# Optimization experiments

Measured on AMD Instinct MI355X. Metric: run time of the kernel, lower is better.

## Reference

```python
import jax, jax.numpy as jnp
import numpy as np

N = 262144   # occupied sparse voxels
C = 64       # channels
K3 = 27      # 3^3 kernel offsets (rulebook width)


def spconv(feats, W, nbr):
    """Submanifold sparse conv: gather -> matmul -> accumulate per kernel offset.
    feats: [N, Cin], W: [K3, Cin, Cout], nbr: [N, K3] int32 neighbor indices.
    """
    def step(acc, wi):
        w, idx = wi          # w: [Cin, Cout], idx: [N]
        return acc + feats[idx] @ w, None
    acc = jnp.zeros((feats.shape[0], W.shape[-1]), dtype=feats.dtype)
    out, _ = jax.lax.scan(step, acc, (W, nbr.T))
    return out


def inr(feats, nbr, w00, w01, w10, w11, w12):
    # branch 0: conv0_1(relu(conv0_0(x)))  (both k=3)
    out0 = spconv(jax.nn.relu(spconv(feats, w00, nbr)), w01, nbr)
    # branch 1: conv1_2(relu(conv1_1(relu(conv1_0(x)))))  (1x1, k=3, 1x1)
    out1 = jax.nn.relu(spconv(jax.nn.relu(feats @ w10), w11, nbr)) @ w12
    # concat halves back to C, residual add
    return jnp.concatenate([out0, out1], axis=1) + feats


def setup_inputs() -> dict:
    key = jax.random.key(0)
    ks = jax.random.split(key, 16)
    Ch = C // 2
    s3 = 1.0 / np.sqrt(K3 * C)
    s3h = 1.0 / np.sqrt(K3 * Ch)
    s1 = 1.0 / np.sqrt(C)
    s1h = 1.0 / np.sqrt(Ch)
    feats = jax.random.normal(ks[0], (N, C), dtype=jnp.float32)
    nbr = jax.random.randint(ks[1], (N, K3), 0, N, dtype=jnp.int32)
    w1 = jax.random.normal(ks[2], (K3, C, C), dtype=jnp.float32) * s3
    w2 = jax.random.normal(ks[3], (K3, C, C), dtype=jnp.float32) * s3
    # 3 stacked INR blocks
    b00 = jax.random.normal(ks[4], (3, K3, C, Ch), dtype=jnp.float32) * s3
    b01 = jax.random.normal(ks[5], (3, K3, Ch, Ch), dtype=jnp.float32) * s3h
    b10 = jax.random.normal(ks[6], (3, C, Ch), dtype=jnp.float32) * s1
    b11 = jax.random.normal(ks[7], (3, K3, Ch, Ch), dtype=jnp.float32) * s3h
    b12 = jax.random.normal(ks[8], (3, Ch, Ch), dtype=jnp.float32) * s1h
    return {"feats": feats, "nbr": nbr, "w1": w1, "w2": w2,
            "b00": b00, "b01": b01, "b10": b10, "b11": b11, "b12": b12}


def reference(feats, nbr, w1, w2, b00, b01, b10, b11, b12):
    x = jax.nn.relu(spconv(feats, w1, nbr))   # x = relu(conv1(x))
    h = x
    for i in range(3):
        h = inr(h, nbr, b00[i], b01[i], b10[i], b11[i], b12[i])
    out = h + x                                # block(x) + x
    return spconv(out, w2, nbr)                # conv2(out)
```

## Files before the change

### kernel.cpp

```cpp
#include <hip/hip_runtime.h>
#include <hip/hip_bf16.h>

typedef __attribute__((ext_vector_type(8))) __bf16 bf16x8;
typedef __attribute__((ext_vector_type(4))) float f32x4;

#define DEVI __device__ __forceinline__

static constexpr int NVOX = 262144;

DEVI unsigned short f2b_rne(float f) {
    unsigned int u = __float_as_uint(f);
    u = (u + 0x7fffu + ((u >> 16) & 1u)) >> 16;
    return (unsigned short)u;
}
DEVI float b2f(unsigned short h) {
    return __uint_as_float(((unsigned int)h) << 16);
}
DEVI bf16x8 ld8(const unsigned short* p) { return *reinterpret_cast<const bf16x8*>(p); }
DEVI f32x4 mfma16(bf16x8 a, bf16x8 b, f32x4 c) {
    return __builtin_amdgcn_mfma_f32_16x16x32_bf16(a, b, c, 0, 0, 0);
}

DEVI void stage16(const unsigned short* __restrict__ src, unsigned short* dst,
                  int n16, int tid, int nthr) {
    const float4* s = reinterpret_cast<const float4*>(src);
    float4* d = reinterpret_cast<float4*>(dst);
    for (int c = tid; c < n16; c += nthr) d[c] = s[c];
}


__global__ void f2b_kernel(const float* __restrict__ src, unsigned short* __restrict__ dst) {
    const size_t i = (size_t)(blockIdx.x * 256 + threadIdx.x) * 8;
    const float4 a = *reinterpret_cast<const float4*>(src + i);
    const float4 b = *reinterpret_cast<const float4*>(src + i + 4);
    union { unsigned short h[8]; uint4 v; } o;
    o.h[0] = f2b_rne(a.x); o.h[1] = f2b_rne(a.y); o.h[2] = f2b_rne(a.z); o.h[3] = f2b_rne(a.w);
    o.h[4] = f2b_rne(b.x); o.h[5] = f2b_rne(b.y); o.h[6] = f2b_rne(b.z); o.h[7] = f2b_rne(b.w);
    *reinterpret_cast<uint4*>(dst + i) = o.v;
}

__global__ void wconv_kernel(const float* __restrict__ src, unsigned short* __restrict__ dst,
                             int K, int Cin, int Cout) {
    const int KC = Cin >> 5, NT = Cout >> 4;
    const int total = K * KC * NT * 512;
    src += (size_t)blockIdx.y * K * Cin * Cout;
    dst += (size_t)blockIdx.y * total;
    for (int e = blockIdx.x * 256 + threadIdx.x; e < total; e += gridDim.x * 256) {
        const int j = e & 7;
        const int ln = (e >> 3) & 63;
        const int blob = e >> 9;
        const int nt = blob % NT;
        const int t = blob / NT;
        const int kc = t % KC;
        const int k = t / KC;
        const int cin = kc * 32 + (ln >> 4) * 8 + j;
        const int cout = nt * 16 + (ln & 15);
        dst[e] = f2b_rne(src[((size_t)k * Cin + cin) * Cout + cout]);
    }
}


template<bool RELU, bool OUTF32>
__global__ __launch_bounds__(1024)
void conv_full_kernel(const unsigned short* __restrict__ in,
                      const int* __restrict__ nbr,
                      const unsigned short* __restrict__ wf,
                      void* __restrict__ outv)
{
    __shared__ unsigned short wlds[14 * 8 * 512];
    const int tid = threadIdx.x;
    const int lane = tid & 63, wave = tid >> 6;
    const int lrow = lane & 15, lkg = lane >> 4;
    const int vb = blockIdx.x * 512 + wave * 32;

    constexpr int ID = 6;
    constexpr int GS = 3;

    const int* nrow0 = nbr + (size_t)(vb + lrow) * 27;
    const int* nrow1 = nbr + (size_t)(vb + 16 + lrow) * 27;

    int i0[ID], i1[ID];
    bf16x8 ga[GS][2][2];

#pragma unroll
    for (int t = 0; t < ID; ++t) { i0[t] = nrow0[t]; i1[t] = nrow1[t]; }
#pragma unroll
    for (int t = 0; t < 2; ++t) {
        const unsigned short* a0 = in + (size_t)i0[t] * 64 + lkg * 8;
        const unsigned short* a1 = in + (size_t)i1[t] * 64 + lkg * 8;
        ga[t][0][0] = ld8(a0); ga[t][0][1] = ld8(a0 + 32);
        ga[t][1][0] = ld8(a1); ga[t][1][1] = ld8(a1 + 32);
    }

    stage16(wf, wlds, 14 * 8 * 64, tid, 1024);

    const f32x4 FZ = {0.f, 0.f, 0.f, 0.f};
    f32x4 acc[2][4];
#pragma unroll
    for (int m = 0; m < 2; ++m)
#pragma unroll
        for (int nt = 0; nt < 4; ++nt) acc[m][nt] = FZ;

    __syncthreads();

#pragma unroll
    for (int t = 0; t < 27; ++t) {
        if (t == 14) {
            __syncthreads();
            stage16(wf + (size_t)14 * 8 * 512, wlds, 13 * 8 * 64, tid, 1024);
            __syncthreads();
        }
        if (t + ID < 27) {
            i0[t % ID] = nrow0[t + ID];
            i1[t % ID] = nrow1[t + ID];
        }
        if (t + 2 < 27) {
            const int u = t + 2, s = u % GS;
            const unsigned short* a0 = in + (size_t)i0[u % ID] * 64 + lkg * 8;
            const unsigned short* a1 = in + (size_t)i1[u % ID] * 64 + lkg * 8;
            ga[s][0][0] = ld8(a0); ga[s][0][1] = ld8(a0 + 32);
            ga[s][1][0] = ld8(a1); ga[s][1][1] = ld8(a1 + 32);
        }
        const int kk = (t < 14) ? t : t - 14;
        const unsigned short* bl = wlds + kk * 8 * 512 + lane * 8;
        const int s = t % GS;
#pragma unroll
        for (int kc = 0; kc < 2; ++kc)
#pragma unroll
            for (int nt = 0; nt < 4; ++nt) {
                const bf16x8 bf = ld8(bl + (kc * 4 + nt) * 512);
                acc[0][nt] = mfma16(ga[s][0][kc], bf, acc[0][nt]);
                acc[1][nt] = mfma16(ga[s][1][kc], bf, acc[1][nt]);
            }
    }

#pragma unroll
    for (int m = 0; m < 2; ++m)
#pragma unroll
        for (int nt = 0; nt < 4; ++nt)
#pragma unroll
            for (int r = 0; r < 4; ++r) {
                const int v = vb + m * 16 + lkg * 4 + r;
                float val = acc[m][nt][r];
                if (RELU) val = fmaxf(val, 0.f);
                if (OUTF32)
                    reinterpret_cast<float*>(outv)[(size_t)v * 64 + nt * 16 + lrow] = val;
                else
                    reinterpret_cast<unsigned short*>(outv)[(size_t)v * 64 + nt * 16 + lrow] = f2b_rne(val);
            }
}

__global__ __launch_bounds__(1024)
void kernel_A(const unsigned short* __restrict__ h,
              const int* __restrict__ nbr,
              const unsigned short* __restrict__ b00f,
              const unsigned short* __restrict__ b10f,
              unsigned short* __restrict__ u)
{
    __shared__ unsigned short wlds[(27 * 4 + 4) * 512];
    const int tid = threadIdx.x;
    const int lane = tid & 63, wave = tid >> 6;
    const int lrow = lane & 15, lkg = lane >> 4;
    const int vb = blockIdx.x * 512 + wave * 32;

    constexpr int ID = 6;
    constexpr int GS = 3;

    const int* nrow0 = nbr + (size_t)(vb + lrow) * 27;
    const int* nrow1 = nbr + (size_t)(vb + 16 + lrow) * 27;

    int i0[ID], i1[ID];
    bf16x8 ga[GS][2][2];

#pragma unroll
    for (int t = 0; t < ID; ++t) { i0[t] = nrow0[t]; i1[t] = nrow1[t]; }
#pragma unroll
    for (int t = 0; t < 2; ++t) {
        const unsigned short* a0 = h + (size_t)i0[t] * 64 + lkg * 8;
        const unsigned short* a1 = h + (size_t)i1[t] * 64 + lkg * 8;
        ga[t][0][0] = ld8(a0); ga[t][0][1] = ld8(a0 + 32);
        ga[t][1][0] = ld8(a1); ga[t][1][1] = ld8(a1 + 32);
    }

    stage16(b00f, wlds, 27 * 4 * 64, tid, 1024);
    stage16(b10f, wlds + 27 * 4 * 512, 4 * 64, tid, 1024);

    const f32x4 FZ = {0.f, 0.f, 0.f, 0.f};
    f32x4 acc0[2][2], acc1[2][2];
#pragma unroll
    for (int m = 0; m < 2; ++m)
#pragma unroll
        for (int nt = 0; nt < 2; ++nt) { acc0[m][nt] = FZ; acc1[m][nt] = FZ; }

    __syncthreads();

#pragma unroll
    for (int t = 0; t < 27; ++t) {
        if (t + ID < 27) {
            i0[t % ID] = nrow0[t + ID];
            i1[t % ID] = nrow1[t + ID];
        }
        if (t + 2 < 27) {
            const int u2 = t + 2, s = u2 % GS;
            const unsigned short* a0 = h + (size_t)i0[u2 % ID] * 64 + lkg * 8;
            const unsigned short* a1 = h + (size_t)i1[u2 % ID] * 64 + lkg * 8;
            ga[s][0][0] = ld8(a0); ga[s][0][1] = ld8(a0 + 32);
            ga[s][1][0] = ld8(a1); ga[s][1][1] = ld8(a1 + 32);
        }
        const unsigned short* bl = wlds + t * 4 * 512 + lane * 8;
        const int s = t % GS;
#pragma unroll
        for (int kc = 0; kc < 2; ++kc)
#pragma unroll
            for (int nt = 0; nt < 2; ++nt) {
                const bf16x8 bf = ld8(bl + (kc * 2 + nt) * 512);
                acc0[0][nt] = mfma16(ga[s][0][kc], bf, acc0[0][nt]);
                acc0[1][nt] = mfma16(ga[s][1][kc], bf, acc0[1][nt]);
            }
    }
    {
        const unsigned short* bl = wlds + 27 * 4 * 512 + lane * 8;
#pragma unroll
        for (int m = 0; m < 2; ++m) {
            const unsigned short* ar = h + (size_t)(vb + m * 16 + lrow) * 64;
#pragma unroll
            for (int kc = 0; kc < 2; ++kc) {
                const bf16x8 af = ld8(ar + kc * 32 + lkg * 8);
#pragma unroll
                for (int nt = 0; nt < 2; ++nt) {
                    const bf16x8 bf = ld8(bl + (kc * 2 + nt) * 512);
                    acc1[m][nt] = mfma16(af, bf, acc1[m][nt]);
                }
            }
        }
    }
#pragma unroll
    for (int m = 0; m < 2; ++m)
#pragma unroll
        for (int nt = 0; nt < 2; ++nt)
#pragma unroll
            for (int r = 0; r < 4; ++r) {
                const int v = vb + m * 16 + lkg * 4 + r;
                u[(size_t)v * 64 + nt * 16 + lrow] = f2b_rne(fmaxf(acc0[m][nt][r], 0.f));
                u[(size_t)v * 64 + 32 + nt * 16 + lrow] = f2b_rne(fmaxf(acc1[m][nt][r], 0.f));
            }
}

__global__ __launch_bounds__(1024)
void kernel_B(const unsigned short* __restrict__ u,
              const int* __restrict__ nbr,
              const unsigned short* __restrict__ b01f,
              const unsigned short* __restrict__ b11f,
              const unsigned short* __restrict__ b12f,
              const unsigned short* __restrict__ hres,
              const unsigned short* __restrict__ xres,
              unsigned short* __restrict__ hout)
{
    __shared__ unsigned short wlds[110 * 512];
    __shared__ unsigned short t2lds[16][512];
    const int tid = threadIdx.x;
    const int lane = tid & 63, wave = tid >> 6;
    const int lrow = lane & 15, lkg = lane >> 4;
    const int vb = blockIdx.x * 512 + wave * 32;

    constexpr int ID = 6;
    constexpr int GS = 3;

    const int* nrow0 = nbr + (size_t)(vb + lrow) * 27;
    const int* nrow1 = nbr + (size_t)(vb + 16 + lrow) * 27;

    int i0[ID], i1[ID];
    bf16x8 ga[GS][2][2];

#pragma unroll
    for (int t = 0; t < ID; ++t) { i0[t] = nrow0[t]; i1[t] = nrow1[t]; }
#pragma unroll
    for (int t = 0; t < 2; ++t) {
        const unsigned short* a0 = u + (size_t)i0[t] * 64 + lkg * 8;
        const unsigned short* a1 = u + (size_t)i1[t] * 64 + lkg * 8;
        ga[t][0][0] = ld8(a0); ga[t][0][1] = ld8(a0 + 32);
        ga[t][1][0] = ld8(a1); ga[t][1][1] = ld8(a1 + 32);
    }

    stage16(b01f, wlds, 54 * 64, tid, 1024);
    stage16(b11f, wlds + 54 * 512, 54 * 64, tid, 1024);
    stage16(b12f, wlds + 108 * 512, 2 * 64, tid, 1024);

    const f32x4 FZ = {0.f, 0.f, 0.f, 0.f};
    f32x4 acc0[2][2], acc1[2][2];
#pragma unroll
    for (int m = 0; m < 2; ++m)
#pragma unroll
        for (int nt = 0; nt < 2; ++nt) { acc0[m][nt] = FZ; acc1[m][nt] = FZ; }

    __syncthreads();

#pragma unroll
    for (int t = 0; t < 27; ++t) {
        if (t + ID < 27) {
            i0[t % ID] = nrow0[t + ID];
            i1[t % ID] = nrow1[t + ID];
        }
        if (t + 2 < 27) {
            const int u2 = t + 2, s = u2 % GS;
            const unsigned short* a0 = u + (size_t)i0[u2 % ID] * 64 + lkg * 8;
            const unsigned short* a1 = u + (size_t)i1[u2 % ID] * 64 + lkg * 8;
            ga[s][0][0] = ld8(a0); ga[s][0][1] = ld8(a0 + 32);
            ga[s][1][0] = ld8(a1); ga[s][1][1] = ld8(a1 + 32);
        }
        const unsigned short* bl = wlds + lane * 8;
        const int s = t % GS;
#pragma unroll
        for (int nt = 0; nt < 2; ++nt) {
            const bf16x8 w01 = ld8(bl + (t * 2 + nt) * 512);
            const bf16x8 w11 = ld8(bl + (54 + t * 2 + nt) * 512);
            acc0[0][nt] = mfma16(ga[s][0][0], w01, acc0[0][nt]);
            acc0[1][nt] = mfma16(ga[s][1][0], w01, acc0[1][nt]);
            acc1[0][nt] = mfma16(ga[s][0][1], w11, acc1[0][nt]);
            acc1[1][nt] = mfma16(ga[s][1][1], w11, acc1[1][nt]);
        }
    }

    f32x4 out1[2][2];
    char* tb = reinterpret_cast<char*>(&t2lds[wave][0]);
#pragma unroll
    for (int m = 0; m < 2; ++m) {
#pragma unroll
        for (int nt = 0; nt < 2; ++nt)
#pragma unroll
            for (int r = 0; r < 4; ++r) {
                const int row = lkg * 4 + r;
                const int byte = (nt * 16 + lrow) * 2;
                const int off = row * 64 + (((byte >> 4) ^ (row & 3)) << 4) + (byte & 15);
                *reinterpret_cast<unsigned short*>(tb + off) = f2b_rne(fmaxf(acc1[m][nt][r], 0.f));
            }
        __syncthreads();
        const int roff = lrow * 64 + ((lkg ^ (lrow & 3)) << 4);
        const bf16x8 af2 = *reinterpret_cast<const bf16x8*>(tb + roff);
#pragma unroll
        for (int nt = 0; nt < 2; ++nt) {
            const bf16x8 w12 = ld8(wlds + (108 + nt) * 512 + lane * 8);
            out1[m][nt] = mfma16(af2, w12, FZ);
        }
        __syncthreads();
    }

#pragma unroll
    for (int m = 0; m < 2; ++m)
#pragma unroll
        for (int nt = 0; nt < 2; ++nt)
#pragma unroll
            for (int r = 0; r < 4; ++r) {
                const int v = vb + m * 16 + lkg * 4 + r;
                const int c0 = nt * 16 + lrow;
                const int c1 = 32 + c0;
                float r0 = acc0[m][nt][r] + b2f(hres[(size_t)v * 64 + c0]);
                float r1 = out1[m][nt][r] + b2f(hres[(size_t)v * 64 + c1]);
                if (xres) {
                    r0 += b2f(xres[(size_t)v * 64 + c0]);
                    r1 += b2f(xres[(size_t)v * 64 + c1]);
                }
                hout[(size_t)v * 64 + c0] = f2b_rne(r0);
                hout[(size_t)v * 64 + c1] = f2b_rne(r1);
            }
}


extern "C" void kernel_launch(void* const* d_in, const int* in_sizes, int n_in,
                              void* d_out, int out_size, void* d_ws, size_t ws_size,
                              hipStream_t stream)
{
    const float* feats = (const float*)d_in[0];
    const int*   nbr   = (const int*)d_in[1];
    const float* w1    = (const float*)d_in[2];
    const float* w2    = (const float*)d_in[3];
    const float* b00   = (const float*)d_in[4];
    const float* b01   = (const float*)d_in[5];
    const float* b10   = (const float*)d_in[6];
    const float* b11   = (const float*)d_in[7];
    const float* b12   = (const float*)d_in[8];

    const size_t NC = (size_t)NVOX * 64;
    unsigned short* xbuf = (unsigned short*)d_ws;
    unsigned short* hbuf = xbuf + NC;
    unsigned short* wbuf = hbuf + NC;
    if (ws_size < (2 * NC + 562176) * sizeof(unsigned short)) return;

    unsigned short* fbuf = (unsigned short*)d_out;
    unsigned short* ubuf = fbuf + NC;

    const size_t OFF_W1 = 0, OFF_W2 = 110592, OFF_B00 = 221184, OFF_B01 = 387072,
                 OFF_B10 = 470016, OFF_B11 = 476160, OFF_B12 = 559104;

    f2b_kernel<<<8192, 256, 0, stream>>>(feats, fbuf);
    wconv_kernel<<<dim3(432, 1), 256, 0, stream>>>(w1, wbuf + OFF_W1, 27, 64, 64);
    wconv_kernel<<<dim3(432, 1), 256, 0, stream>>>(w2, wbuf + OFF_W2, 27, 64, 64);
    wconv_kernel<<<dim3(216, 3), 256, 0, stream>>>(b00, wbuf + OFF_B00, 27, 64, 32);
    wconv_kernel<<<dim3(108, 3), 256, 0, stream>>>(b01, wbuf + OFF_B01, 27, 32, 32);
    wconv_kernel<<<dim3(8, 3),   256, 0, stream>>>(b10, wbuf + OFF_B10, 1, 64, 32);
    wconv_kernel<<<dim3(108, 3), 256, 0, stream>>>(b11, wbuf + OFF_B11, 27, 32, 32);
    wconv_kernel<<<dim3(4, 3),   256, 0, stream>>>(b12, wbuf + OFF_B12, 1, 32, 32);

    conv_full_kernel<true, false><<<512, 1024, 0, stream>>>(fbuf, nbr, wbuf + OFF_W1, xbuf);

    for (int i = 0; i < 3; ++i) {
        kernel_A<<<512, 1024, 0, stream>>>(i ? hbuf : xbuf, nbr,
                                           wbuf + OFF_B00 + (size_t)i * 55296,
                                           wbuf + OFF_B10 + (size_t)i * 2048, ubuf);
        kernel_B<<<512, 1024, 0, stream>>>(ubuf, nbr,
                                           wbuf + OFF_B01 + (size_t)i * 27648,
                                           wbuf + OFF_B11 + (size_t)i * 27648,
                                           wbuf + OFF_B12 + (size_t)i * 1024,
                                           i ? hbuf : xbuf,
                                           (i == 2) ? xbuf : (const unsigned short*)nullptr,
                                           hbuf);
    }

    conv_full_kernel<false, true><<<512, 1024, 0, stream>>>(hbuf, nbr, wbuf + OFF_W2, d_out);
}
```

Baseline: 1.174 ms.

## Shrink LDS weight footprint with chunked staging to raise occupancy

Each conv kernel now stages its weights into LDS in smaller chunks (7 offsets, or two halves of 14 and 13) instead of the whole 27-offset set, and kernel_B reuses the weight buffer as its transpose scratch and reads the 1x1 weights from global memory into registers. Launch bounds now request more waves per EU. The aim is to cut per-block LDS use so more 1024-thread blocks fit per CU and hide gather latency better. The cost is extra barriers and restaging inside the main loop, which stall every wave while a chunk loads, plus tighter register limits that could cause spills.

```diff
diff --git a/kernel.cpp b/kernel.cpp
--- a/kernel.cpp
+++ b/kernel.cpp
@@ -61,13 +61,13 @@
 
 
 template<bool RELU, bool OUTF32>
-__global__ __launch_bounds__(1024)
+__global__ __launch_bounds__(1024, 8)
 void conv_full_kernel(const unsigned short* __restrict__ in,
                       const int* __restrict__ nbr,
                       const unsigned short* __restrict__ wf,
                       void* __restrict__ outv)
 {
-    __shared__ unsigned short wlds[14 * 8 * 512];
+    __shared__ unsigned short wlds[7 * 8 * 512];
     const int tid = threadIdx.x;
     const int lane = tid & 63, wave = tid >> 6;
     const int lrow = lane & 15, lkg = lane >> 4;
@@ -92,8 +92,6 @@
         ga[t][1][0] = ld8(a1); ga[t][1][1] = ld8(a1 + 32);
     }
 
-    stage16(wf, wlds, 14 * 8 * 64, tid, 1024);
-
     const f32x4 FZ = {0.f, 0.f, 0.f, 0.f};
     f32x4 acc[2][4];
 #pragma unroll
@@ -101,13 +99,12 @@
 #pragma unroll
         for (int nt = 0; nt < 4; ++nt) acc[m][nt] = FZ;
 
-    __syncthreads();
-
 #pragma unroll
     for (int t = 0; t < 27; ++t) {
-        if (t == 14) {
-            __syncthreads();
-            stage16(wf + (size_t)14 * 8 * 512, wlds, 13 * 8 * 64, tid, 1024);
+        if (t % 7 == 0) {
+            const int nk = (27 - t) < 7 ? (27 - t) : 7;
+            __syncthreads();
+            stage16(wf + (size_t)t * 8 * 512, wlds, nk * 8 * 64, tid, 1024);
             __syncthreads();
         }
         if (t + ID < 27) {
@@ -121,7 +118,7 @@
             ga[s][0][0] = ld8(a0); ga[s][0][1] = ld8(a0 + 32);
             ga[s][1][0] = ld8(a1); ga[s][1][1] = ld8(a1 + 32);
         }
-        const int kk = (t < 14) ? t : t - 14;
+        const int kk = t % 7;
         const unsigned short* bl = wlds + kk * 8 * 512 + lane * 8;
         const int s = t % GS;
 #pragma unroll
@@ -150,14 +147,14 @@
             }
 }
 
-__global__ __launch_bounds__(1024)
+__global__ __launch_bounds__(1024, 8)
 void kernel_A(const unsigned short* __restrict__ h,
               const int* __restrict__ nbr,
               const unsigned short* __restrict__ b00f,
               const unsigned short* __restrict__ b10f,
               unsigned short* __restrict__ u)
 {
-    __shared__ unsigned short wlds[(27 * 4 + 4) * 512];
+    __shared__ unsigned short wlds[60 * 512];
     const int tid = threadIdx.x;
     const int lane = tid & 63, wave = tid >> 6;
     const int lrow = lane & 15, lkg = lane >> 4;
@@ -182,9 +179,6 @@
         ga[t][1][0] = ld8(a1); ga[t][1][1] = ld8(a1 + 32);
     }
 
-    stage16(b00f, wlds, 27 * 4 * 64, tid, 1024);
-    stage16(b10f, wlds + 27 * 4 * 512, 4 * 64, tid, 1024);
-
     const f32x4 FZ = {0.f, 0.f, 0.f, 0.f};
     f32x4 acc0[2][2], acc1[2][2];
 #pragma unroll
@@ -192,10 +186,18 @@
 #pragma unroll
         for (int nt = 0; nt < 2; ++nt) { acc0[m][nt] = FZ; acc1[m][nt] = FZ; }
 
-    __syncthreads();
-
 #pragma unroll
     for (int t = 0; t < 27; ++t) {
+        if (t == 0) {
+            __syncthreads();
+            stage16(b00f, wlds, 14 * 4 * 64, tid, 1024);
+            stage16(b10f, wlds + 56 * 512, 4 * 64, tid, 1024);
+            __syncthreads();
+        } else if (t == 14) {
+            __syncthreads();
+            stage16(b00f + (size_t)14 * 4 * 512, wlds, 13 * 4 * 64, tid, 1024);
+            __syncthreads();
+        }
         if (t + ID < 27) {
             i0[t % ID] = nrow0[t + ID];
             i1[t % ID] = nrow1[t + ID];
@@ -207,7 +209,8 @@
             ga[s][0][0] = ld8(a0); ga[s][0][1] = ld8(a0 + 32);
             ga[s][1][0] = ld8(a1); ga[s][1][1] = ld8(a1 + 32);
         }
-        const unsigned short* bl = wlds + t * 4 * 512 + lane * 8;
+        const int kk = (t < 14) ? t : t - 14;
+        const unsigned short* bl = wlds + kk * 4 * 512 + lane * 8;
         const int s = t % GS;
 #pragma unroll
         for (int kc = 0; kc < 2; ++kc)
@@ -219,7 +222,7 @@
             }
     }
     {
-        const unsigned short* bl = wlds + 27 * 4 * 512 + lane * 8;
+        const unsigned short* bl = wlds + 56 * 512 + lane * 8;
 #pragma unroll
         for (int m = 0; m < 2; ++m) {
             const unsigned short* ar = h + (size_t)(vb + m * 16 + lrow) * 64;
@@ -246,7 +249,7 @@
             }
 }
 
-__global__ __launch_bounds__(1024)
+__global__ __launch_bounds__(1024, 8)
 void kernel_B(const unsigned short* __restrict__ u,
               const int* __restrict__ nbr,
               const unsigned short* __restrict__ b01f,
@@ -256,8 +259,7 @@
               const unsigned short* __restrict__ xres,
               unsigned short* __restrict__ hout)
 {
-    __shared__ unsigned short wlds[110 * 512];
-    __shared__ unsigned short t2lds[16][512];
+    __shared__ unsigned short wlds[56 * 512];
     const int tid = threadIdx.x;
     const int lane = tid & 63, wave = tid >> 6;
     const int lrow = lane & 15, lkg = lane >> 4;
@@ -282,10 +284,6 @@
         ga[t][1][0] = ld8(a1); ga[t][1][1] = ld8(a1 + 32);
     }
 
-    stage16(b01f, wlds, 54 * 64, tid, 1024);
-    stage16(b11f, wlds + 54 * 512, 54 * 64, tid, 1024);
-    stage16(b12f, wlds + 108 * 512, 2 * 64, tid, 1024);
-
     const f32x4 FZ = {0.f, 0.f, 0.f, 0.f};
     f32x4 acc0[2][2], acc1[2][2];
 #pragma unroll
@@ -293,10 +291,19 @@
 #pragma unroll
         for (int nt = 0; nt < 2; ++nt) { acc0[m][nt] = FZ; acc1[m][nt] = FZ; }
 
-    __syncthreads();
-
 #pragma unroll
     for (int t = 0; t < 27; ++t) {
+        if (t == 0) {
+            __syncthreads();
+            stage16(b01f, wlds, 14 * 2 * 64, tid, 1024);
+            stage16(b11f, wlds + 28 * 512, 14 * 2 * 64, tid, 1024);
+            __syncthreads();
+        } else if (t == 14) {
+            __syncthreads();
+            stage16(b01f + (size_t)28 * 512, wlds, 13 * 2 * 64, tid, 1024);
+            stage16(b11f + (size_t)28 * 512, wlds + 28 * 512, 13 * 2 * 64, tid, 1024);
+            __syncthreads();
+        }
         if (t + ID < 27) {
             i0[t % ID] = nrow0[t + ID];
             i1[t % ID] = nrow1[t + ID];
@@ -308,12 +315,13 @@
             ga[s][0][0] = ld8(a0); ga[s][0][1] = ld8(a0 + 32);
             ga[s][1][0] = ld8(a1); ga[s][1][1] = ld8(a1 + 32);
         }
+        const int kk = (t < 14) ? t : t - 14;
         const unsigned short* bl = wlds + lane * 8;
         const int s = t % GS;
 #pragma unroll
         for (int nt = 0; nt < 2; ++nt) {
-            const bf16x8 w01 = ld8(bl + (t * 2 + nt) * 512);
-            const bf16x8 w11 = ld8(bl + (54 + t * 2 + nt) * 512);
+            const bf16x8 w01 = ld8(bl + (kk * 2 + nt) * 512);
+            const bf16x8 w11 = ld8(bl + (28 + kk * 2 + nt) * 512);
             acc0[0][nt] = mfma16(ga[s][0][0], w01, acc0[0][nt]);
             acc0[1][nt] = mfma16(ga[s][1][0], w01, acc0[1][nt]);
             acc1[0][nt] = mfma16(ga[s][0][1], w11, acc1[0][nt]);
@@ -321,8 +329,14 @@
         }
     }
 
+    bf16x8 w12r[2];
+#pragma unroll
+    for (int nt = 0; nt < 2; ++nt) w12r[nt] = ld8(b12f + nt * 512 + lane * 8);
+
+    __syncthreads();
+
     f32x4 out1[2][2];
-    char* tb = reinterpret_cast<char*>(&t2lds[wave][0]);
+    char* tb = reinterpret_cast<char*>(wlds) + wave * 1024;
 #pragma unroll
     for (int m = 0; m < 2; ++m) {
 #pragma unroll
@@ -338,10 +352,8 @@
         const int roff = lrow * 64 + ((lkg ^ (lrow & 3)) << 4);
         const bf16x8 af2 = *reinterpret_cast<const bf16x8*>(tb + roff);
 #pragma unroll
-        for (int nt = 0; nt < 2; ++nt) {
-            const bf16x8 w12 = ld8(wlds + (108 + nt) * 512 + lane * 8);
-            out1[m][nt] = mfma16(af2, w12, FZ);
-        }
+        for (int nt = 0; nt < 2; ++nt)
+            out1[m][nt] = mfma16(af2, w12r[nt], FZ);
         __syncthreads();
     }
 
```

Measured after the change: 1.994 ms. 1.7x slower.
